# Kernel tuning notes

Hardware: AMD Instinct MI355X
Metric: run time of the kernel (lower is better)

## Reference

```python
import jax, jax.numpy as jnp
import numpy as np

B, S, HID = 2, 2048, 2048
NH, NKV, HD = 16, 4, 128
MAXPOS = 2048


def _rope_tables(features, length, max_timescale=10000.0):
    fraction = jnp.arange(0, features, 2, dtype=jnp.float32) / features
    inv_freq = 1.0 / (max_timescale ** fraction)
    sinusoid = jnp.einsum('i,j->ij', jnp.arange(length, dtype=jnp.float32), inv_freq)
    sinusoid = jnp.concatenate([sinusoid, sinusoid], axis=-1)  # [length, features]
    return jnp.sin(sinusoid), jnp.cos(sinusoid)


def rotate_half(x):
    x1, x2 = jnp.split(x, 2, axis=-1)
    return jnp.concatenate([-x2, x1], axis=-1)


def setup_inputs() -> dict:
    key = jax.random.key(0)
    k1, k2, k3, k4, k5 = jax.random.split(key, 5)
    scale = 1.0 / np.sqrt(HID)
    hidden_states = jax.random.normal(k1, (B, S, HID), dtype=jnp.float32)
    Wq = jax.random.normal(k2, (NH * HD, HID), dtype=jnp.float32) * scale
    Wk = jax.random.normal(k3, (NKV * HD, HID), dtype=jnp.float32) * scale
    Wv = jax.random.normal(k4, (NKV * HD, HID), dtype=jnp.float32) * scale
    Wo = jax.random.normal(k5, (HID, NH * HD), dtype=jnp.float32) * scale
    # causal additive mask [B,1,S,S]
    neg = jnp.finfo(jnp.float32).min
    causal = jnp.where(jnp.tril(jnp.ones((S, S), dtype=bool)), 0.0, neg)
    attention_mask = jnp.broadcast_to(causal[None, None], (B, 1, S, S))
    sin, cos = _rope_tables(HD, MAXPOS)
    return {"hidden_states": hidden_states, "attention_mask": attention_mask,
            "Wq": Wq, "Wk": Wk, "Wv": Wv, "Wo": Wo, "sin": sin, "cos": cos}


def reference(hidden_states, attention_mask, Wq, Wk, Wv, Wo, sin, cos):
    bsz, qlen, _ = hidden_states.shape
    # projections (Linear, no bias): x @ W.T -> [B,S,heads,hd]
    q = (hidden_states @ Wq.T).reshape(bsz, qlen, NH, HD)
    k = (hidden_states @ Wk.T).reshape(bsz, qlen, NKV, HD)
    v = (hidden_states @ Wv.T).reshape(bsz, qlen, NKV, HD)
    # rotary embedding (applied in [B,S,H,D] layout)
    qcos = cos[:qlen][None, :, None, :]
    qsin = sin[:qlen][None, :, None, :]
    q = q * qcos + rotate_half(q) * qsin
    k = k * qcos + rotate_half(k) * qsin
    # GQA: repeat_kv equivalent via einsum grouping; expand kv heads to NH
    n_rep = NH // NKV
    q_g = q.reshape(bsz, qlen, NKV, n_rep, HD)  # group queries per kv head
    # scores: NOTE original applies no 1/sqrt(d) scaling
    scores = jnp.einsum('bqhrd,bkhd->bhrqk', q_g, k).reshape(bsz, NH, qlen, qlen)
    mask = attention_mask.at[:, :, :, 0].set(0.0)
    scores = scores + mask
    probs = jax.nn.softmax(scores.astype(jnp.float32), axis=-1).astype(q.dtype)
    probs_g = probs.reshape(bsz, NKV, n_rep, qlen, qlen)
    out = jnp.einsum('bhrqk,bkhd->bqhrd', probs_g, v).reshape(bsz, qlen, NH * HD)
    return out @ Wo.T
```

## Files before the change

### kernel.cpp

```cpp
#include <hip/hip_runtime.h>
#include <hip/hip_bf16.h>

typedef _Float16 f16x8 __attribute__((ext_vector_type(8)));
typedef __fp16 h16x2 __attribute__((ext_vector_type(2)));
typedef float f32x4 __attribute__((ext_vector_type(4)));
typedef float f32x16 __attribute__((ext_vector_type(16)));

#define B_    2
#define S_    2048
#define HID_  2048
#define NH_   16
#define NKV_  4
#define HD_   128
#define M_TOK 4096
#define NQKV  3072

#define MFMA16(a, b, c) __builtin_amdgcn_mfma_f32_16x16x32_f16(a, b, c, 0, 0, 0)
#define MFMA32(a, b, c) __builtin_amdgcn_mfma_f32_32x32x16_f16(a, b, c, 0, 0, 0)

union UW { unsigned u; h16x2 h; };

__device__ __forceinline__ unsigned short f2h(float f) {
  _Float16 h = (_Float16)f;
  return *(unsigned short*)&h;
}

__device__ __forceinline__ void gload_lds16(const unsigned short* g, unsigned short* l) {
  __builtin_amdgcn_global_load_lds((const __attribute__((address_space(1))) void*)g,
                                   (__attribute__((address_space(3))) void*)l,
                                   16, 0, 0);
}

__global__ void cast_f32_f16(const float* __restrict__ src, unsigned short* __restrict__ dst, int n4) {
  int i = blockIdx.x * blockDim.x + threadIdx.x;
  int stride = gridDim.x * blockDim.x;
  for (int idx = i; idx < n4; idx += stride) {
    float4 v = reinterpret_cast<const float4*>(src)[idx];
    ushort4 o;
    o.x = f2h(v.x); o.y = f2h(v.y); o.z = f2h(v.z); o.w = f2h(v.w);
    reinterpret_cast<ushort4*>(dst)[idx] = o;
  }
}

#define BM 128
#define BN 128
#define BK 32

__global__ __launch_bounds__(256) void gemm_bt_f16(
    const unsigned short* __restrict__ A, const unsigned short* __restrict__ Bm,
    float* __restrict__ C, int M, int N, int K) {
  __shared__ unsigned short As[BM * BK];
  __shared__ unsigned short Bs[BN * BK];
  const int tid  = threadIdx.x;
  const int lane = tid & 63;
  const int wave = tid >> 6;
  const int nbn  = N / BN;
  const int brow = (blockIdx.x / nbn) * BM;
  const int bcol = (blockIdx.x % nbn) * BN;
  const int wr = (wave >> 1) * 64;
  const int wc = (wave & 1) * 64;

  const int srow = wave * 16 + (lane >> 2);
  const int scol = (lane & 3) * 8;
  const unsigned short* ag = A + (size_t)(brow + srow) * K + scol;
  const unsigned short* bg = Bm + (size_t)(bcol + srow) * K + scol;
  unsigned short* aldsw = As + wave * 512;
  unsigned short* bldsw = Bs + wave * 512;

  f32x4 acc[4][4];
#pragma unroll
  for (int m = 0; m < 4; ++m)
#pragma unroll
    for (int n = 0; n < 4; ++n) acc[m][n] = (f32x4){0.f, 0.f, 0.f, 0.f};

  const int lr = lane & 15;
  const int lg = lane >> 4;

  for (int kt = 0; kt < K; kt += BK) {
    __syncthreads();
    gload_lds16(ag + kt, aldsw);
    gload_lds16(ag + (size_t)64 * K + kt, aldsw + 2048);
    gload_lds16(bg + kt, bldsw);
    gload_lds16(bg + (size_t)64 * K + kt, bldsw + 2048);
    __syncthreads();
    f16x8 af[4], bfr[4];
#pragma unroll
    for (int m = 0; m < 4; ++m)
      af[m] = *reinterpret_cast<const f16x8*>(&As[(wr + m * 16 + lr) * BK + lg * 8]);
#pragma unroll
    for (int n = 0; n < 4; ++n)
      bfr[n] = *reinterpret_cast<const f16x8*>(&Bs[(wc + n * 16 + lr) * BK + lg * 8]);
#pragma unroll
    for (int m = 0; m < 4; ++m)
#pragma unroll
      for (int n = 0; n < 4; ++n)
        acc[m][n] = MFMA16(af[m], bfr[n], acc[m][n]);
  }

#pragma unroll
  for (int m = 0; m < 4; ++m) {
#pragma unroll
    for (int r = 0; r < 4; ++r) {
      int row = brow + wr + m * 16 + lg * 4 + r;
      float* cp = C + (size_t)row * N + bcol + wc + lr;
#pragma unroll
      for (int n = 0; n < 4; ++n) cp[n * 16] = acc[m][n][r];
    }
  }
}

__global__ void rope_relayout(const float* __restrict__ QKV,
                              const float* __restrict__ sin_t, const float* __restrict__ cos_t,
                              unsigned short* __restrict__ Qo, unsigned short* __restrict__ Ko,
                              unsigned short* __restrict__ Vt) {
  int idx = blockIdx.x * blockDim.x + threadIdx.x;
  int d  = idx & 63;
  int t  = idx >> 6;
  int hh = t % 24;
  int bs = t / 24;
  int s  = bs & (S_ - 1);
  int b  = bs >> 11;
  const float* xrow = QKV + (size_t)bs * NQKV;
  if (hh < 16) {
    float x0 = xrow[hh * 128 + d], x1 = xrow[hh * 128 + 64 + d];
    float c = cos_t[s * 128 + d], sn = sin_t[s * 128 + d];
    unsigned short* qp = Qo + (((size_t)(b * 16 + hh) * S_) + s) * 128 + d;
    qp[0]  = f2h(x0 * c - x1 * sn);
    qp[64] = f2h(x1 * c + x0 * sn);
  } else if (hh < 20) {
    int kvh = hh - 16;
    float x0 = xrow[2048 + kvh * 128 + d], x1 = xrow[2048 + kvh * 128 + 64 + d];
    float c = cos_t[s * 128 + d], sn = sin_t[s * 128 + d];
    unsigned short* kp = Ko + (((size_t)(b * 4 + kvh) * S_) + s) * 128 + d;
    kp[0]  = f2h(x0 * c - x1 * sn);
    kp[64] = f2h(x1 * c + x0 * sn);
  } else {
    int kvh = hh - 20;
    float x0 = xrow[2560 + kvh * 128 + d], x1 = xrow[2560 + kvh * 128 + 64 + d];
    unsigned short* vp = Vt + ((size_t)(b * 4 + kvh) * 128 + d) * S_ + s;
    vp[0]        = f2h(x0);
    vp[64 * S_]  = f2h(x1);
  }
}

__global__ __launch_bounds__(256, 2) void flash_attn6(
    const unsigned short* __restrict__ Q, const unsigned short* __restrict__ Kk,
    const unsigned short* __restrict__ Vt, unsigned short* __restrict__ Ao) {
  __shared__ _Float16 Kl[2][64 * 128];
  __shared__ _Float16 Vl[2][128 * 64];
  const int lane = threadIdx.x & 63;
  const int w    = threadIdx.x >> 6;
  const int bh   = blockIdx.x & 31;
  const int bq   = 15 - (int)(blockIdx.x >> 5);
  const int b    = bh >> 4, h = bh & 15, kvh = h >> 2;
  const int q31  = lane & 31;
  const int hi   = lane >> 5;
  const int qb   = bq * 128;
  const int wqb  = qb + w * 32;
  const int qrow = wqb + q31;

  const _Float16* Qp = (const _Float16*)Q + (((size_t)(b * 16 + h) * S_) + qrow) * 128;
  const _Float16* Kp = (const _Float16*)Kk + ((size_t)(b * 4 + kvh) * S_) * 128;
  const _Float16* Vp = (const _Float16*)Vt + ((size_t)(b * 4 + kvh) * 128) * S_;

  f16x8 qf[8];
#pragma unroll
  for (int s = 0; s < 8; ++s) {
    f16x8 t = *reinterpret_cast<const f16x8*>(Qp + s * 16 + hi * 8);
#pragma unroll
    for (int j = 0; j < 8; ++j) t[j] = (_Float16)((float)t[j] * 1.44269504f);
    qf[s] = t;
  }

  f32x16 po0 = {}, po1 = {}, po2 = {}, po3 = {};
  float m = -1e30f, l = 0.f;

  const int krow = (lane >> 4);
  const int vrow = (lane >> 3);
  const int wklim = wqb + 32;
  const int nt = qb / 64 + 2;

#define STAGE(K0S, BUF)                                                               \
  {                                                                                   \
    unsigned short* kdst = (unsigned short*)Kl[BUF] + w * 2048;                       \
    unsigned short* vdst = (unsigned short*)Vl[BUF] + w * 2048;                       \
    _Pragma("unroll") for (int jj = 0; jj < 4; ++jj) {                                \
      const int j = w * 4 + jj;                                                       \
      const int kr = j * 4 + krow;                                                    \
      const int kc = (lane & 15) ^ (kr & 7);                                          \
      gload_lds16((const unsigned short*)(Kp + (size_t)((K0S) + kr) * 128 + kc * 8),  \
                  kdst + jj * 512);                                                   \
      const int vr = j * 8 + vrow;                                                    \
      const int vc = (lane & 7) ^ (vr & 7);                                           \
      gload_lds16((const unsigned short*)(Vp + (size_t)vr * S_ + (K0S) + vc * 8),     \
                  vdst + jj * 512);                                                   \
    }                                                                                 \
  }

  STAGE(0, 0)
  __syncthreads();

  int cur = 0;
  const int r7 = q31 & 7;
  for (int t = 0; t < nt; ++t) {
    const int k0 = t * 64;
    if (t + 1 < nt) STAGE((t + 1) * 64, cur ^ 1)

    if (k0 < wklim) {
      f32x16 s0 = {}, s1 = {};
      const _Float16* Kc = Kl[cur];
      __builtin_amdgcn_s_setprio(1);
#pragma unroll
      for (int s = 0; s < 8; ++s) {
        const int cc = (hi + 2 * s) ^ r7;
        f16x8 kf0 = *reinterpret_cast<const f16x8*>(Kc + q31 * 128 + cc * 8);
        f16x8 kf1 = *reinterpret_cast<const f16x8*>(Kc + (q31 + 32) * 128 + cc * 8);
        s0 = MFMA32(kf0, qf[s], s0);
        s1 = MFMA32(kf1, qf[s], s1);
      }
      __builtin_amdgcn_s_setprio(0);

      if (k0 + 63 > wqb) {
        int qrel = qrow - k0 - 4 * hi;
#pragma unroll
        for (int r = 0; r < 16; ++r) {
          int cr = (r & 3) + 8 * (r >> 2);
          if (cr > qrel)      s0[r] = -1e30f;
          if (cr + 32 > qrel) s1[r] = -1e30f;
        }
      }
      float pmax = s0[0];
#pragma unroll
      for (int r = 1; r < 16; ++r) pmax = fmaxf(pmax, s0[r]);
#pragma unroll
      for (int r = 0; r < 16; ++r) pmax = fmaxf(pmax, s1[r]);
      pmax = fmaxf(pmax, __shfl_xor(pmax, 32));
      if (__any(pmax > m + 8.0f)) {
        float mn = fmaxf(m, pmax);
        float sc = __builtin_amdgcn_exp2f(m - mn);
        l *= sc;
#pragma unroll
        for (int r = 0; r < 16; ++r) {
          po0[r] *= sc; po1[r] *= sc; po2[r] *= sc; po3[r] *= sc;
        }
        m = mn;
      }
      float rs = 0.f;
#pragma unroll
      for (int r = 0; r < 16; ++r) { s0[r] = __builtin_amdgcn_exp2f(s0[r] - m); rs += s0[r]; }
#pragma unroll
      for (int r = 0; r < 16; ++r) { s1[r] = __builtin_amdgcn_exp2f(s1[r] - m); rs += s1[r]; }
      l += rs + __shfl_xor(rs, 32);

      f16x8 pa[4];
#pragma unroll
      for (int sl = 0; sl < 4; ++sl) {
        f32x16 sv = (sl < 2) ? s0 : s1;
        const int R = (sl & 1) * 8;
        UW w00, w01, w10, w11;
        w00.h = __builtin_amdgcn_cvt_pkrtz(sv[R + 0], sv[R + 1]);
        w01.h = __builtin_amdgcn_cvt_pkrtz(sv[R + 2], sv[R + 3]);
        w10.h = __builtin_amdgcn_cvt_pkrtz(sv[R + 4], sv[R + 5]);
        w11.h = __builtin_amdgcn_cvt_pkrtz(sv[R + 6], sv[R + 7]);
        unsigned x00 = __shfl_xor(w00.u, 32);
        unsigned x01 = __shfl_xor(w01.u, 32);
        unsigned x10 = __shfl_xor(w10.u, 32);
        unsigned x11 = __shfl_xor(w11.u, 32);
        UW W0, W1, W2, W3;
        W0.u = hi ? x10 : w00.u;
        W1.u = hi ? x11 : w01.u;
        W2.u = hi ? w10.u : x00;
        W3.u = hi ? w11.u : x01;
        union { unsigned uu[4]; f16x8 v; } pk;
        pk.uu[0] = W0.u; pk.uu[1] = W1.u; pk.uu[2] = W2.u; pk.uu[3] = W3.u;
        pa[sl] = pk.v;
      }

      const _Float16* Vc = Vl[cur];
      __builtin_amdgcn_s_setprio(1);
#pragma unroll
      for (int s = 0; s < 4; ++s) {
        const int cc = (hi + 2 * s) ^ r7;
        f16x8 vf0 = *reinterpret_cast<const f16x8*>(Vc + q31 * 64 + cc * 8);
        po0 = MFMA32(vf0, pa[s], po0);
        f16x8 vf1 = *reinterpret_cast<const f16x8*>(Vc + (q31 + 32) * 64 + cc * 8);
        po1 = MFMA32(vf1, pa[s], po1);
        f16x8 vf2 = *reinterpret_cast<const f16x8*>(Vc + (q31 + 64) * 64 + cc * 8);
        po2 = MFMA32(vf2, pa[s], po2);
        f16x8 vf3 = *reinterpret_cast<const f16x8*>(Vc + (q31 + 96) * 64 + cc * 8);
        po3 = MFMA32(vf3, pa[s], po3);
      }
      __builtin_amdgcn_s_setprio(0);
    }

    __syncthreads();
    cur ^= 1;
  }
#undef STAGE

  float inv = 1.0f / l;
  unsigned short* orow = Ao + ((size_t)(b * S_ + qrow)) * 2048 + h * 128;
#define STORE_DB(PO, DB)                                                          \
  {                                                                               \
    _Pragma("unroll") for (int a4 = 0; a4 < 4; ++a4) {                            \
      UW e0, e1;                                                                  \
      e0.h = __builtin_amdgcn_cvt_pkrtz(PO[4 * a4 + 0] * inv, PO[4 * a4 + 1] * inv); \
      e1.h = __builtin_amdgcn_cvt_pkrtz(PO[4 * a4 + 2] * inv, PO[4 * a4 + 3] * inv); \
      unsigned long long pv = ((unsigned long long)e1.u << 32) | e0.u;            \
      *reinterpret_cast<unsigned long long*>(orow + DB * 32 + a4 * 8 + hi * 4) = pv; \
    }                                                                             \
  }
  STORE_DB(po0, 0)
  STORE_DB(po1, 1)
  STORE_DB(po2, 2)
  STORE_DB(po3, 3)
#undef STORE_DB
}

extern "C" void kernel_launch(void* const* d_in, const int* in_sizes, int n_in,
                              void* d_out, int out_size, void* d_ws, size_t ws_size,
                              hipStream_t stream) {
  const float* hs    = (const float*)d_in[0];
  const float* Wq    = (const float*)d_in[2];
  const float* Wk    = (const float*)d_in[3];
  const float* Wv    = (const float*)d_in[4];
  const float* Wo    = (const float*)d_in[5];
  const float* sin_t = (const float*)d_in[6];
  const float* cos_t = (const float*)d_in[7];

  char* ws = (char*)d_ws;
  unsigned short* Xb    = (unsigned short*)ws; ws += (size_t)M_TOK * HID_ * 2;
  unsigned short* Wqkvb = (unsigned short*)ws; ws += (size_t)NQKV * HID_ * 2;
  unsigned short* Wob   = (unsigned short*)ws; ws += (size_t)HID_ * HID_ * 2;
  float*          QKV   = (float*)ws;          ws += (size_t)M_TOK * NQKV * 4;
  unsigned short* Qb    = (unsigned short*)ws; ws += (size_t)B_ * NH_ * S_ * HD_ * 2;
  unsigned short* Kb    = (unsigned short*)ws; ws += (size_t)B_ * NKV_ * S_ * HD_ * 2;
  unsigned short* Vtb   = (unsigned short*)ws; ws += (size_t)B_ * NKV_ * S_ * HD_ * 2;
  unsigned short* Aob   = (unsigned short*)ws; ws += (size_t)M_TOK * HID_ * 2;

  cast_f32_f16<<<2048, 256, 0, stream>>>(hs, Xb, M_TOK * HID_ / 4);
  cast_f32_f16<<<1024, 256, 0, stream>>>(Wq, Wqkvb, 2048 * 2048 / 4);
  cast_f32_f16<<<512,  256, 0, stream>>>(Wk, Wqkvb + 2048 * 2048, 512 * 2048 / 4);
  cast_f32_f16<<<512,  256, 0, stream>>>(Wv, Wqkvb + 2560 * 2048, 512 * 2048 / 4);
  cast_f32_f16<<<1024, 256, 0, stream>>>(Wo, Wob, 2048 * 2048 / 4);

  gemm_bt_f16<<<(M_TOK / BM) * (NQKV / BN), 256, 0, stream>>>(Xb, Wqkvb, QKV, M_TOK, NQKV, HID_);

  rope_relayout<<<(B_ * S_ * 24 * 64) / 256, 256, 0, stream>>>(QKV, sin_t, cos_t, Qb, Kb, Vtb);

  flash_attn6<<<512, 256, 0, stream>>>(Qb, Kb, Vtb, Aob);

  gemm_bt_f16<<<(M_TOK / BM) * (HID_ / BN), 256, 0, stream>>>(Aob, Wob, (float*)d_out, M_TOK, HID_, HID_);
}
```

Before: 260.6 us.

## Replace GEMM with 256x256-tile double-buffered swizzled LDS kernel

Both projection GEMMs move from a 128x128 tile, 4-wave kernel with BK=32 to a 256x256 tile, 8-wave kernel with BK=64. The new kernel double-buffers A and B in LDS using async global-to-LDS loads with an XOR swizzle, and splits each K step into four compute phases with barriers and raised wave priority. It also remaps block IDs across groups of 8 for locality. The aim is more reuse per loaded byte, overlap of loads with MFMA work, and fewer LDS bank conflicts. The tradeoff is a much smaller grid (192 and 128 blocks) on a device with many CUs, plus 128KB of LDS per block, which limits occupancy.

After: 287.3 us. 1.1x slower.

```diff
diff --git a/kernel.cpp b/kernel.cpp
--- a/kernel.cpp
+++ b/kernel.cpp
@@ -42,67 +42,108 @@
   }
 }
 
-#define BM 128
-#define BN 128
-#define BK 32
-
-__global__ __launch_bounds__(256) void gemm_bt_f16(
+__global__ __launch_bounds__(512, 2) void gemm8p_f16(
     const unsigned short* __restrict__ A, const unsigned short* __restrict__ Bm,
     float* __restrict__ C, int M, int N, int K) {
-  __shared__ unsigned short As[BM * BK];
-  __shared__ unsigned short Bs[BN * BK];
+  __shared__ unsigned short Asb[2][256 * 64];
+  __shared__ unsigned short Bsb[2][256 * 64];
   const int tid  = threadIdx.x;
   const int lane = tid & 63;
-  const int wave = tid >> 6;
-  const int nbn  = N / BN;
-  const int brow = (blockIdx.x / nbn) * BM;
-  const int bcol = (blockIdx.x % nbn) * BN;
-  const int wr = (wave >> 1) * 64;
-  const int wc = (wave & 1) * 64;
-
-  const int srow = wave * 16 + (lane >> 2);
-  const int scol = (lane & 3) * 8;
-  const unsigned short* ag = A + (size_t)(brow + srow) * K + scol;
-  const unsigned short* bg = Bm + (size_t)(bcol + srow) * K + scol;
-  unsigned short* aldsw = As + wave * 512;
-  unsigned short* bldsw = Bs + wave * 512;
-
-  f32x4 acc[4][4];
-#pragma unroll
-  for (int m = 0; m < 4; ++m)
+  const int wid  = tid >> 6;
+  const int wm = wid >> 2, wn = wid & 3;
+  const int lr = lane & 15, lg = lane >> 4;
+
+  const int nbn = N >> 8;
+  const int cpx = ((M >> 8) * nbn) >> 3;
+  int bid = (int)blockIdx.x;
+  bid = (bid & 7) * cpx + (bid >> 3);
+  const int brow = (bid / nbn) << 8;
+  const int bcol = (bid % nbn) << 8;
+
+#define G8_STAGE(KT, BUF)                                                            \
+  {                                                                                  \
+    _Pragma("unroll") for (int ch = 0; ch < 4; ++ch) {                               \
+      const int G = ch * 512 + tid;                                                  \
+      const int r = G >> 3, g = G & 7;                                               \
+      const int gc = g ^ (r & 7);                                                    \
+      gload_lds16(A + (size_t)(brow + r) * K + (KT) + gc * 8,                        \
+                  &Asb[BUF][(ch * 512 + wid * 64) * 8]);                             \
+    }                                                                                \
+    _Pragma("unroll") for (int ch = 0; ch < 4; ++ch) {                               \
+      const int G = ch * 512 + tid;                                                  \
+      const int r = G >> 3, g = G & 7;                                               \
+      const int gc = g ^ (r & 7);                                                    \
+      gload_lds16(Bm + (size_t)(bcol + r) * K + (KT) + gc * 8,                       \
+                  &Bsb[BUF][(ch * 512 + wid * 64) * 8]);                             \
+    }                                                                                \
+  }
+
+  f32x4 acc[8][4];
+#pragma unroll
+  for (int m = 0; m < 8; ++m)
 #pragma unroll
     for (int n = 0; n < 4; ++n) acc[m][n] = (f32x4){0.f, 0.f, 0.f, 0.f};
 
-  const int lr = lane & 15;
-  const int lg = lane >> 4;
-
-  for (int kt = 0; kt < K; kt += BK) {
-    __syncthreads();
-    gload_lds16(ag + kt, aldsw);
-    gload_lds16(ag + (size_t)64 * K + kt, aldsw + 2048);
-    gload_lds16(bg + kt, bldsw);
-    gload_lds16(bg + (size_t)64 * K + kt, bldsw + 2048);
-    __syncthreads();
-    f16x8 af[4], bfr[4];
-#pragma unroll
-    for (int m = 0; m < 4; ++m)
-      af[m] = *reinterpret_cast<const f16x8*>(&As[(wr + m * 16 + lr) * BK + lg * 8]);
-#pragma unroll
-    for (int n = 0; n < 4; ++n)
-      bfr[n] = *reinterpret_cast<const f16x8*>(&Bs[(wc + n * 16 + lr) * BK + lg * 8]);
-#pragma unroll
-    for (int m = 0; m < 4; ++m)
-#pragma unroll
-      for (int n = 0; n < 4; ++n)
-        acc[m][n] = MFMA16(af[m], bfr[n], acc[m][n]);
-  }
-
-#pragma unroll
-  for (int m = 0; m < 4; ++m) {
+  const int nk = K >> 6;
+  G8_STAGE(0, 0)
+  G8_STAGE(64, 1)
+  asm volatile("s_waitcnt vmcnt(8)" ::: "memory");
+  __builtin_amdgcn_s_barrier();
+
+  for (int t = 0; t < nk; ++t) {
+    const unsigned short* Ac = Asb[t & 1];
+    const unsigned short* Bc = Bsb[t & 1];
+#pragma unroll
+    for (int ph = 0; ph < 4; ++ph) {
+      const int qm = ph >> 1, qn = ph & 1;
+      f16x8 af[4][2], bf[2][2];
+#pragma unroll
+      for (int m2 = 0; m2 < 4; ++m2)
+#pragma unroll
+        for (int ks = 0; ks < 2; ++ks) {
+          const int row = wm * 128 + (qm * 4 + m2) * 16 + lr;
+          const int gs = (ks * 4 + lg) ^ (row & 7);
+          af[m2][ks] = *reinterpret_cast<const f16x8*>(Ac + row * 64 + gs * 8);
+        }
+#pragma unroll
+      for (int n2 = 0; n2 < 2; ++n2)
+#pragma unroll
+        for (int ks = 0; ks < 2; ++ks) {
+          const int row = wn * 64 + (qn * 2 + n2) * 16 + lr;
+          const int gs = (ks * 4 + lg) ^ (row & 7);
+          bf[n2][ks] = *reinterpret_cast<const f16x8*>(Bc + row * 64 + gs * 8);
+        }
+      __builtin_amdgcn_s_barrier();
+      asm volatile("s_waitcnt lgkmcnt(0)" ::: "memory");
+      __builtin_amdgcn_sched_barrier(0);
+      __builtin_amdgcn_s_setprio(1);
+#pragma unroll
+      for (int ks = 0; ks < 2; ++ks)
+#pragma unroll
+        for (int m2 = 0; m2 < 4; ++m2)
+#pragma unroll
+          for (int n2 = 0; n2 < 2; ++n2)
+            acc[qm * 4 + m2][qn * 2 + n2] =
+                MFMA16(af[m2][ks], bf[n2][ks], acc[qm * 4 + m2][qn * 2 + n2]);
+      __builtin_amdgcn_s_setprio(0);
+      __builtin_amdgcn_s_barrier();
+    }
+    if (t + 2 < nk) {
+      G8_STAGE((t + 2) * 64, t & 1)
+      asm volatile("s_waitcnt vmcnt(8)" ::: "memory");
+    } else {
+      asm volatile("s_waitcnt vmcnt(0)" ::: "memory");
+    }
+    __builtin_amdgcn_s_barrier();
+  }
+#undef G8_STAGE
+
+#pragma unroll
+  for (int m = 0; m < 8; ++m) {
 #pragma unroll
     for (int r = 0; r < 4; ++r) {
-      int row = brow + wr + m * 16 + lg * 4 + r;
-      float* cp = C + (size_t)row * N + bcol + wc + lr;
+      const int row = brow + wm * 128 + m * 16 + lg * 4 + r;
+      float* cp = C + (size_t)row * N + bcol + wn * 64 + lr;
 #pragma unroll
       for (int n = 0; n < 4; ++n) cp[n * 16] = acc[m][n][r];
     }
@@ -344,11 +385,11 @@
   cast_f32_f16<<<512,  256, 0, stream>>>(Wv, Wqkvb + 2560 * 2048, 512 * 2048 / 4);
   cast_f32_f16<<<1024, 256, 0, stream>>>(Wo, Wob, 2048 * 2048 / 4);
 
-  gemm_bt_f16<<<(M_TOK / BM) * (NQKV / BN), 256, 0, stream>>>(Xb, Wqkvb, QKV, M_TOK, NQKV, HID_);
+  gemm8p_f16<<<(M_TOK / 256) * (NQKV / 256), 512, 0, stream>>>(Xb, Wqkvb, QKV, M_TOK, NQKV, HID_);
 
   rope_relayout<<<(B_ * S_ * 24 * 64) / 256, 256, 0, stream>>>(QKV, sin_t, cos_t, Qb, Kb, Vtb);
 
   flash_attn6<<<512, 256, 0, stream>>>(Qb, Kb, Vtb, Aob);
 
-  gemm_bt_f16<<<(M_TOK / BM) * (HID_ / BN), 256, 0, stream>>>(Aob, Wob, (float*)d_out, M_TOK, HID_, HID_);
-}
+  gemm8p_f16<<<(M_TOK / 256) * (HID_ / 256), 512, 0, stream>>>(Aob, Wob, (float*)d_out, M_TOK, HID_, HID_);
+}
```
